# Performance work log

Measured on AMD Instinct MI355X. Metric: run time of the kernel, lower is better.

## Reference

```python
import jax, jax.numpy as jnp
import numpy as np

B, C, H, W = 8, 256, 64, 64
CK = 64  # C // k with k=4


def setup_inputs() -> dict:
    key = jax.random.key(0)
    ks = jax.random.split(key, 5)
    s = 1.0 / np.sqrt(C)
    return {
        "x": jax.random.normal(ks[0], (B, C, H, W), dtype=jnp.float32),
        "wq": jax.random.normal(ks[1], (CK, C), dtype=jnp.float32) * s,
        "bq": jnp.zeros((CK,), dtype=jnp.float32),
        "wk": jax.random.normal(ks[2], (CK, C), dtype=jnp.float32) * s,
        "bk": jnp.zeros((CK,), dtype=jnp.float32),
        "wv": jax.random.normal(ks[3], (C, C), dtype=jnp.float32) * s,
        "bv": jnp.zeros((C,), dtype=jnp.float32),
        "wg": jax.random.normal(ks[4], (C, C), dtype=jnp.float32) * s,
        "bg": jnp.zeros((C,), dtype=jnp.float32),
    }


def reference(x, wq, bq, wk, bk, wv, bv, wg, bg):
    b, c, h, w = x.shape
    n = h * w
    xf = x.reshape(b, c, n)  # [B, C, N]
    # 1x1 convs are channel-wise matmuls
    q = jnp.einsum('oc,bcn->bon', wq, xf) + bq[None, :, None]  # [B, Ck, N]
    k = jnp.einsum('oc,bcn->bon', wk, xf) + bk[None, :, None]  # [B, Ck, N]
    v = jnp.einsum('oc,bcn->bon', wv, xf) + bv[None, :, None]  # [B, C, N]
    # energy[b,i,j] = q[b,:,i] . k[b,:,j]
    energy = jnp.einsum('bci,bcj->bij', q, k)  # [B, N, N]
    energy = jax.nn.elu(energy) / n
    out = jnp.einsum('bcn,bnj->bcj', v, energy).reshape(b, c, h, w)
    out = jnp.einsum('oc,bchw->bohw', wg, out) + bg[None, :, None, None]
    return out
```

## Files before the change

kernel.cpp:

```cpp
#include <hip/hip_runtime.h>
#include <math.h>

#define BATCH 8
#define CH    256
#define NPIX  4096
#define CKDIM 64

typedef __attribute__((ext_vector_type(8))) short short8;
typedef __attribute__((ext_vector_type(4))) float f32x4;

#define MFMA16x16(a, b, c) __builtin_amdgcn_mfma_f32_16x16x32_bf16((a), (b), (c), 0, 0, 0)

__device__ __forceinline__ unsigned short f2bf(float f) {
    union { float f; unsigned int u; } v; v.f = f;
    unsigned int u = v.u;
    u += 0x7fffu + ((u >> 16) & 1u);
    return (unsigned short)(u >> 16);
}

__global__ void prep_kernel(const float* __restrict__ wq, const float* __restrict__ bq,
                            const float* __restrict__ wk, const float* __restrict__ bk,
                            const float* __restrict__ wv, const float* __restrict__ bv,
                            const float* __restrict__ wg,
                            unsigned short* __restrict__ W_all, float* __restrict__ bias_all) {
    int o = blockIdx.x;
    int c = threadIdx.x;
    if (o < 64) {
        W_all[o * CH + c] = f2bf(wq[o * CH + c]);
        if (c == 0) bias_all[o] = bq[o];
    } else if (o < 128) {
        int oo = o - 64;
        W_all[o * CH + c] = f2bf(wk[oo * CH + c]);
        if (c == 0) bias_all[o] = bk[oo];
    } else {
        int oo = o - 128;
        float acc = 0.f;
        for (int m = 0; m < CH; ++m)
            acc += wg[oo * CH + m] * wv[m * CH + c];
        W_all[o * CH + c] = f2bf(acc);
        if (c == 0) {
            float b = 0.f;
            for (int m = 0; m < CH; ++m) b += wg[oo * CH + m] * bv[m];
            bias_all[o] = b;
        }
    }
}

__global__ void xpose_kernel(const float* __restrict__ x, unsigned short* __restrict__ xt) {
    __shared__ float Tl[64][65];
    int n0 = blockIdx.x * 64;
    int c0 = blockIdx.y * 64;
    int b  = blockIdx.z;
    int tid = threadIdx.x;

#pragma unroll
    for (int r = 0; r < 4; ++r) {
        int f  = r * 256 + tid;
        int c  = f >> 4;
        int n4 = f & 15;
        float4 v = *(const float4*)(x + ((size_t)b * CH + c0 + c) * NPIX + n0 + n4 * 4);
        Tl[n4 * 4 + 0][c] = v.x;
        Tl[n4 * 4 + 1][c] = v.y;
        Tl[n4 * 4 + 2][c] = v.z;
        Tl[n4 * 4 + 3][c] = v.w;
    }
    __syncthreads();
#pragma unroll
    for (int r = 0; r < 2; ++r) {
        int f    = r * 256 + tid;
        int nrow = f >> 3;
        int c8   = f & 7;
        unsigned int pk[4];
#pragma unroll
        for (int p = 0; p < 4; ++p) {
            unsigned int lo = f2bf(Tl[nrow][c8 * 8 + p * 2 + 0]);
            unsigned int hi = f2bf(Tl[nrow][c8 * 8 + p * 2 + 1]);
            pk[p] = lo | (hi << 16);
        }
        *(uint4*)(xt + ((size_t)b * NPIX + n0 + nrow) * CH + c0 + c8 * 8) = *(uint4*)pk;
    }
}

__global__ void qkv_mfma(const unsigned short* __restrict__ xt,
                         const unsigned short* __restrict__ W_all,
                         const float* __restrict__ bias_all,
                         unsigned short* __restrict__ qk, unsigned short* __restrict__ vp) {
    __shared__ __align__(16) unsigned short Xl[64][264];

    int n0   = blockIdx.x * 64;
    int b    = blockIdx.y;
    int tid  = threadIdx.x;
    int lane = tid & 63;
    int w    = tid >> 6;
    int col  = lane & 15;
    int quad = lane >> 4;

#pragma unroll
    for (int r = 0; r < 8; ++r) {
        int f   = r * 256 + tid;
        int row = f >> 5;
        int c8  = f & 31;
        *(uint4*)&Xl[row][c8 * 8] = *(const uint4*)(xt + ((size_t)b * NPIX + n0 + row) * CH + c8 * 8);
    }
    __syncthreads();

#pragma unroll
    for (int og = 0; og < 6; ++og) {
        int o0 = og * 64;
        const unsigned short* Arow = W_all + (size_t)(o0 + w * 16 + col) * CH + quad * 8;

        f32x4 acc[4];
#pragma unroll
        for (int t = 0; t < 4; ++t) acc[t] = (f32x4){0.f, 0.f, 0.f, 0.f};

#pragma unroll
        for (int kc = 0; kc < 8; ++kc) {
            short8 a = *(const short8*)(Arow + kc * 32);
#pragma unroll
            for (int nt = 0; nt < 4; ++nt) {
                short8 bb = *(const short8*)&Xl[nt * 16 + col][kc * 32 + quad * 8];
                acc[nt] = MFMA16x16(a, bb, acc[nt]);
            }
        }

        float4 bias = *(const float4*)(bias_all + o0 + w * 16 + quad * 4);
        float bs[4] = {bias.x, bias.y, bias.z, bias.w};

        if (og < 2) {
#pragma unroll
            for (int nt = 0; nt < 4; ++nt) {
                int n = n0 + nt * 16 + col;
                unsigned int pk[2];
#pragma unroll
                for (int p = 0; p < 2; ++p) {
                    unsigned int lo = f2bf(acc[nt][p * 2 + 0] + bs[p * 2 + 0]);
                    unsigned int hi = f2bf(acc[nt][p * 2 + 1] + bs[p * 2 + 1]);
                    pk[p] = lo | (hi << 16);
                }
                *(uint2*)(qk + ((size_t)b * NPIX + n) * 128 + o0 + w * 16 + quad * 4) = *(uint2*)pk;
            }
        } else {
#pragma unroll
            for (int nt = 0; nt < 4; ++nt) {
                int n = n0 + nt * 16 + col;
#pragma unroll
                for (int r = 0; r < 4; ++r) {
                    int oo = o0 - 128 + w * 16 + quad * 4 + r;
                    vp[((size_t)b * CH + oo) * NPIX + n] = f2bf(acc[nt][r] + bs[r]);
                }
            }
        }
    }
}

#define LPK 72
__global__ __launch_bounds__(512, 4)
void attn_v4(const unsigned short* __restrict__ qk,
             const unsigned short* __restrict__ vp,
             const float* __restrict__ bg, float* __restrict__ out) {
    __shared__ __align__(16) unsigned short Qt[64][LPK];
    __shared__ __align__(16) unsigned short Vl[256][LPK];
    __shared__ __align__(16) unsigned short St[64][LPK];

    int j0   = blockIdx.x * 64;
    int b    = blockIdx.y;
    int tid  = threadIdx.x;
    int lane = tid & 63;
    int w    = tid >> 6;
    int col  = lane & 15;
    int quad = lane >> 4;

    int tjA = w & 3;
    int tiP = (w >> 2) * 2;

    short8 bK[2];
#pragma unroll
    for (int ks = 0; ks < 2; ++ks)
        bK[ks] = *(const short8*)(qk + ((size_t)b * NPIX + j0 + tjA * 16 + col) * 128 + 64 + ks * 32 + quad * 8);

    f32x4 acc[2][4];
#pragma unroll
    for (int ot = 0; ot < 2; ++ot)
#pragma unroll
        for (int tj = 0; tj < 4; ++tj) acc[ot][tj] = (f32x4){0.f, 0.f, 0.f, 0.f};

    for (int i0 = 0; i0 < NPIX; i0 += 64) {
        __syncthreads();

        {
            int row = tid >> 3, q8 = tid & 7;
            *(uint4*)&Qt[row][q8 * 8] =
                *(const uint4*)(qk + ((size_t)b * NPIX + i0 + row) * 128 + q8 * 8);
        }
#pragma unroll
        for (int r = 0; r < 4; ++r) {
            int f = r * 512 + tid;
            int row = f >> 3, q8 = f & 7;
            *(uint4*)&Vl[row][q8 * 8] =
                *(const uint4*)(vp + ((size_t)b * CH + row) * NPIX + i0 + q8 * 8);
        }
        __syncthreads();

#pragma unroll
        for (int t = 0; t < 2; ++t) {
            int ti = tiP + t;
            short8 a0 = *(const short8*)&Qt[ti * 16 + col][quad * 8];
            short8 a1 = *(const short8*)&Qt[ti * 16 + col][32 + quad * 8];
            f32x4 s = (f32x4){0.f, 0.f, 0.f, 0.f};
            s = MFMA16x16(a0, bK[0], s);
            s = MFMA16x16(a1, bK[1], s);
            unsigned int pk[2];
#pragma unroll
            for (int p = 0; p < 2; ++p) {
                float e0 = s[p * 2 + 0];
                float e1 = s[p * 2 + 1];
                e0 = (e0 > 0.f) ? e0 : (__expf(e0) - 1.f);
                e1 = (e1 > 0.f) ? e1 : (__expf(e1) - 1.f);
                e0 *= (1.f / (float)NPIX);
                e1 *= (1.f / (float)NPIX);
                pk[p] = (unsigned int)f2bf(e0) | ((unsigned int)f2bf(e1) << 16);
            }
            *(uint2*)&St[tjA * 16 + col][ti * 16 + quad * 4] = *(uint2*)pk;
        }
        __syncthreads();

#pragma unroll
        for (int ks = 0; ks < 2; ++ks) {
            short8 sb[4];
#pragma unroll
            for (int tj = 0; tj < 4; ++tj)
                sb[tj] = *(const short8*)&St[tj * 16 + col][ks * 32 + quad * 8];
#pragma unroll
            for (int ot = 0; ot < 2; ++ot) {
                short8 bv = *(const short8*)&Vl[(w * 2 + ot) * 16 + col][ks * 32 + quad * 8];
#pragma unroll
                for (int tj = 0; tj < 4; ++tj)
                    acc[ot][tj] = MFMA16x16(sb[tj], bv, acc[ot][tj]);
            }
        }
    }

#pragma unroll
    for (int ot = 0; ot < 2; ++ot) {
        int o = (w * 2 + ot) * 16 + col;
        float bgv = bg[o];
#pragma unroll
        for (int tj = 0; tj < 4; ++tj) {
            int j = j0 + tj * 16 + quad * 4;
            float4 st;
            st.x = acc[ot][tj][0] + bgv;
            st.y = acc[ot][tj][1] + bgv;
            st.z = acc[ot][tj][2] + bgv;
            st.w = acc[ot][tj][3] + bgv;
            *(float4*)&out[((size_t)b * CH + o) * NPIX + j] = st;
        }
    }
}

extern "C" void kernel_launch(void* const* d_in, const int* in_sizes, int n_in,
                              void* d_out, int out_size, void* d_ws, size_t ws_size,
                              hipStream_t stream) {
    const float* x  = (const float*)d_in[0];
    const float* wq = (const float*)d_in[1];
    const float* bq = (const float*)d_in[2];
    const float* wk = (const float*)d_in[3];
    const float* bk = (const float*)d_in[4];
    const float* wv = (const float*)d_in[5];
    const float* bv = (const float*)d_in[6];
    const float* wg = (const float*)d_in[7];
    const float* bg = (const float*)d_in[8];
    float* out = (float*)d_out;

    unsigned short* W_all = (unsigned short*)d_ws;
    float* bias_all = (float*)(W_all + 384 * 256);
    unsigned short* xt = (unsigned short*)(bias_all + 384);
    unsigned short* qk = xt + (size_t)BATCH * NPIX * CH;
    unsigned short* vp = qk + (size_t)BATCH * NPIX * 128;

    prep_kernel<<<dim3(384), dim3(256), 0, stream>>>(wq, bq, wk, bk, wv, bv, wg, W_all, bias_all);
    xpose_kernel<<<dim3(NPIX / 64, CH / 64, BATCH), dim3(256), 0, stream>>>(x, xt);
    qkv_mfma<<<dim3(NPIX / 64, BATCH), dim3(256), 0, stream>>>(xt, W_all, bias_all, qk, vp);
    attn_v4<<<dim3(NPIX / 64, BATCH), dim3(512), 0, stream>>>(qk, vp, bg, out);
}
```

Measured before the change: 265.9 us.

## Widen attention tile to 128 columns with double-buffered register-staged prefetch

The attention kernel now covers 128 output columns per block instead of 64. Each wave accumulates a 64x64 output tile, which halves how often the V and Q tiles are reloaded per output. The next Q/V tile is prefetched into registers during compute and written to a second LDS buffer, hiding global load latency. It also uses a hardware packed bf16 convert, a branch-free ELU, and raised wave priority around the MFMA loop. The cost is higher register and LDS use, with occupancy lowered to 2 blocks per CU, and only 256 blocks in the grid.

```diff
diff --git a/kernel.cpp b/kernel.cpp
--- a/kernel.cpp
+++ b/kernel.cpp
@@ -154,15 +154,15 @@
 }
 
 #define LPK 72
-__global__ __launch_bounds__(512, 4)
-void attn_v4(const unsigned short* __restrict__ qk,
+__global__ __launch_bounds__(512, 2)
+void attn_v5(const unsigned short* __restrict__ qk,
              const unsigned short* __restrict__ vp,
              const float* __restrict__ bg, float* __restrict__ out) {
-    __shared__ __align__(16) unsigned short Qt[64][LPK];
-    __shared__ __align__(16) unsigned short Vl[256][LPK];
-    __shared__ __align__(16) unsigned short St[64][LPK];
-
-    int j0   = blockIdx.x * 64;
+    __shared__ __align__(16) unsigned short Qt[2][64][LPK];
+    __shared__ __align__(16) unsigned short Vl[2][256][LPK];
+    __shared__ __align__(16) unsigned short St[128][LPK];
+
+    int j0   = blockIdx.x * 128;
     int b    = blockIdx.y;
     int tid  = threadIdx.x;
     int lane = tid & 63;
@@ -170,57 +170,85 @@
     int col  = lane & 15;
     int quad = lane >> 4;
 
-    int tjA = w & 3;
-    int tiP = (w >> 2) * 2;
-
-    short8 bK[2];
-#pragma unroll
-    for (int ks = 0; ks < 2; ++ks)
-        bK[ks] = *(const short8*)(qk + ((size_t)b * NPIX + j0 + tjA * 16 + col) * 128 + 64 + ks * 32 + quad * 8);
-
-    f32x4 acc[2][4];
-#pragma unroll
-    for (int ot = 0; ot < 2; ++ot)
-#pragma unroll
-        for (int tj = 0; tj < 4; ++tj) acc[ot][tj] = (f32x4){0.f, 0.f, 0.f, 0.f};
-
-    for (int i0 = 0; i0 < NPIX; i0 += 64) {
-        __syncthreads();
-
-        {
-            int row = tid >> 3, q8 = tid & 7;
-            *(uint4*)&Qt[row][q8 * 8] =
-                *(const uint4*)(qk + ((size_t)b * NPIX + i0 + row) * 128 + q8 * 8);
-        }
+    int wo  = w >> 1;
+    int wj  = w & 1;
+    int paj = w >> 1;
+    int pai = w & 1;
+
+    short8 bK[2][2];
+#pragma unroll
+    for (int jj = 0; jj < 2; ++jj) {
+        int jrow = j0 + (paj * 2 + jj) * 16 + col;
+#pragma unroll
+        for (int ks = 0; ks < 2; ++ks)
+            bK[jj][ks] = *(const short8*)(qk + ((size_t)b * NPIX + jrow) * 128 + 64 + ks * 32 + quad * 8);
+    }
+
+    f32x4 acc[4][4];
+#pragma unroll
+    for (int ot = 0; ot < 4; ++ot)
+#pragma unroll
+        for (int jt = 0; jt < 4; ++jt) acc[ot][jt] = (f32x4){0.f, 0.f, 0.f, 0.f};
+
+    {
+        int row = tid >> 3, q8 = tid & 7;
+        uint4 q0 = *(const uint4*)(qk + ((size_t)b * NPIX + row) * 128 + q8 * 8);
+        *(uint4*)&Qt[0][row][q8 * 8] = q0;
 #pragma unroll
         for (int r = 0; r < 4; ++r) {
             int f = r * 512 + tid;
-            int row = f >> 3, q8 = f & 7;
-            *(uint4*)&Vl[row][q8 * 8] =
-                *(const uint4*)(vp + ((size_t)b * CH + row) * NPIX + i0 + q8 * 8);
-        }
+            uint4 v0 = *(const uint4*)(vp + ((size_t)b * CH + (f >> 3)) * NPIX + (f & 7) * 8);
+            *(uint4*)&Vl[0][f >> 3][(f & 7) * 8] = v0;
+        }
+    }
+
+    const float invN = 1.f / (float)NPIX;
+    uint4 vr[4]; uint4 qr;
+
+    for (int it = 0; it < NPIX / 64; ++it) {
+        int p = it & 1;
+        int more = (it + 1) < (NPIX / 64);
+        int inext = (it + 1) * 64;
+
+        if (more) {
+            int row = tid >> 3, q8 = tid & 7;
+            qr = *(const uint4*)(qk + ((size_t)b * NPIX + inext + row) * 128 + q8 * 8);
+#pragma unroll
+            for (int r = 0; r < 4; ++r) {
+                int f = r * 512 + tid;
+                vr[r] = *(const uint4*)(vp + ((size_t)b * CH + (f >> 3)) * NPIX + inext + (f & 7) * 8);
+            }
+        }
+
         __syncthreads();
 
 #pragma unroll
-        for (int t = 0; t < 2; ++t) {
-            int ti = tiP + t;
-            short8 a0 = *(const short8*)&Qt[ti * 16 + col][quad * 8];
-            short8 a1 = *(const short8*)&Qt[ti * 16 + col][32 + quad * 8];
-            f32x4 s = (f32x4){0.f, 0.f, 0.f, 0.f};
-            s = MFMA16x16(a0, bK[0], s);
-            s = MFMA16x16(a1, bK[1], s);
-            unsigned int pk[2];
-#pragma unroll
-            for (int p = 0; p < 2; ++p) {
-                float e0 = s[p * 2 + 0];
-                float e1 = s[p * 2 + 1];
-                e0 = (e0 > 0.f) ? e0 : (__expf(e0) - 1.f);
-                e1 = (e1 > 0.f) ? e1 : (__expf(e1) - 1.f);
-                e0 *= (1.f / (float)NPIX);
-                e1 *= (1.f / (float)NPIX);
-                pk[p] = (unsigned int)f2bf(e0) | ((unsigned int)f2bf(e1) << 16);
-            }
-            *(uint2*)&St[tjA * 16 + col][ti * 16 + quad * 4] = *(uint2*)pk;
+        for (int ii = 0; ii < 2; ++ii) {
+            int isub = pai * 2 + ii;
+            short8 a0 = *(const short8*)&Qt[p][isub * 16 + col][quad * 8];
+            short8 a1 = *(const short8*)&Qt[p][isub * 16 + col][32 + quad * 8];
+#pragma unroll
+            for (int jj = 0; jj < 2; ++jj) {
+                f32x4 s = (f32x4){0.f, 0.f, 0.f, 0.f};
+                s = MFMA16x16(a0, bK[jj][0], s);
+                s = MFMA16x16(a1, bK[jj][1], s);
+                unsigned int pk2[2];
+#pragma unroll
+                for (int pp = 0; pp < 2; ++pp) {
+                    float e0 = s[pp * 2 + 0];
+                    float e1 = s[pp * 2 + 1];
+                    float g0 = __expf(e0) - 1.f;
+                    float g1 = __expf(e1) - 1.f;
+                    e0 = (e0 > 0.f) ? e0 : g0;
+                    e1 = (e1 > 0.f) ? e1 : g1;
+                    e0 *= invN;
+                    e1 *= invN;
+                    unsigned int rpk;
+                    asm("v_cvt_pk_bf16_f32 %0, %1, %2" : "=v"(rpk) : "v"(e0), "v"(e1));
+                    pk2[pp] = rpk;
+                }
+                *(uint2*)&St[(paj * 2 + jj) * 16 + col][isub * 16 + quad * 4] = *(uint2*)pk2;
+            }
         }
         __syncthreads();
 
@@ -228,30 +256,43 @@
         for (int ks = 0; ks < 2; ++ks) {
             short8 sb[4];
 #pragma unroll
-            for (int tj = 0; tj < 4; ++tj)
-                sb[tj] = *(const short8*)&St[tj * 16 + col][ks * 32 + quad * 8];
-#pragma unroll
-            for (int ot = 0; ot < 2; ++ot) {
-                short8 bv = *(const short8*)&Vl[(w * 2 + ot) * 16 + col][ks * 32 + quad * 8];
-#pragma unroll
-                for (int tj = 0; tj < 4; ++tj)
-                    acc[ot][tj] = MFMA16x16(sb[tj], bv, acc[ot][tj]);
-            }
-        }
-    }
-
-#pragma unroll
-    for (int ot = 0; ot < 2; ++ot) {
-        int o = (w * 2 + ot) * 16 + col;
+            for (int jt = 0; jt < 4; ++jt)
+                sb[jt] = *(const short8*)&St[wj * 64 + jt * 16 + col][ks * 32 + quad * 8];
+#pragma unroll
+            for (int ot = 0; ot < 4; ++ot) {
+                short8 vb = *(const short8*)&Vl[p][wo * 64 + ot * 16 + col][ks * 32 + quad * 8];
+                __builtin_amdgcn_s_setprio(1);
+#pragma unroll
+                for (int jt = 0; jt < 4; ++jt)
+                    acc[ot][jt] = MFMA16x16(sb[jt], vb, acc[ot][jt]);
+                __builtin_amdgcn_s_setprio(0);
+            }
+        }
+
+        if (more) {
+            int pn = p ^ 1;
+            int row = tid >> 3, q8 = tid & 7;
+            *(uint4*)&Qt[pn][row][q8 * 8] = qr;
+#pragma unroll
+            for (int r = 0; r < 4; ++r) {
+                int f = r * 512 + tid;
+                *(uint4*)&Vl[pn][f >> 3][(f & 7) * 8] = vr[r];
+            }
+        }
+    }
+
+#pragma unroll
+    for (int ot = 0; ot < 4; ++ot) {
+        int o = wo * 64 + ot * 16 + col;
         float bgv = bg[o];
 #pragma unroll
-        for (int tj = 0; tj < 4; ++tj) {
-            int j = j0 + tj * 16 + quad * 4;
+        for (int jt = 0; jt < 4; ++jt) {
+            int j = j0 + wj * 64 + jt * 16 + quad * 4;
             float4 st;
-            st.x = acc[ot][tj][0] + bgv;
-            st.y = acc[ot][tj][1] + bgv;
-            st.z = acc[ot][tj][2] + bgv;
-            st.w = acc[ot][tj][3] + bgv;
+            st.x = acc[ot][jt][0] + bgv;
+            st.y = acc[ot][jt][1] + bgv;
+            st.z = acc[ot][jt][2] + bgv;
+            st.w = acc[ot][jt][3] + bgv;
             *(float4*)&out[((size_t)b * CH + o) * NPIX + j] = st;
         }
     }
@@ -280,5 +321,5 @@
     prep_kernel<<<dim3(384), dim3(256), 0, stream>>>(wq, bq, wk, bk, wv, bv, wg, W_all, bias_all);
     xpose_kernel<<<dim3(NPIX / 64, CH / 64, BATCH), dim3(256), 0, stream>>>(x, xt);
     qkv_mfma<<<dim3(NPIX / 64, BATCH), dim3(256), 0, stream>>>(xt, W_all, bias_all, qk, vp);
-    attn_v4<<<dim3(NPIX / 64, BATCH), dim3(512), 0, stream>>>(qk, vp, bg, out);
-}
+    attn_v5<<<dim3(NPIX / 128, BATCH), dim3(512), 0, stream>>>(qk, vp, bg, out);
+}
```

Measured after the change: 305.5 us. 14.9% more time.

## Prefetch Q and V into registers, drop V LDS staging, interleave batch blocks

Applied to the files above, without the earlier changes.

The attention kernel no longer stages V through shared memory. Each lane loads its own V MFMA operand fragments straight from global memory into registers, and the next tile's Q and V are prefetched into registers while the current tile is computed, which removes one barrier per iteration. Block indices are remapped so consecutive blocks cover different batches, the ELU conversion uses the hardware packed bf16 convert with branchless exp, and s_setprio is raised around the MFMA burst. These changes cut LDS traffic and expose load latency overlap, at the cost of higher register pressure and uncoalesced per-lane global V loads.

```diff
diff --git a/kernel.cpp b/kernel.cpp
--- a/kernel.cpp
+++ b/kernel.cpp
@@ -155,15 +155,15 @@
 
 #define LPK 72
 __global__ __launch_bounds__(512, 4)
-void attn_v4(const unsigned short* __restrict__ qk,
+void attn_v6(const unsigned short* __restrict__ qk,
              const unsigned short* __restrict__ vp,
              const float* __restrict__ bg, float* __restrict__ out) {
     __shared__ __align__(16) unsigned short Qt[64][LPK];
-    __shared__ __align__(16) unsigned short Vl[256][LPK];
     __shared__ __align__(16) unsigned short St[64][LPK];
 
-    int j0   = blockIdx.x * 64;
-    int b    = blockIdx.y;
+    int lin  = blockIdx.y * gridDim.x + blockIdx.x;
+    int b    = lin & 7;
+    int j0   = (lin >> 3) * 64;
     int tid  = threadIdx.x;
     int lane = tid & 63;
     int w    = tid >> 6;
@@ -184,21 +184,35 @@
 #pragma unroll
         for (int tj = 0; tj < 4; ++tj) acc[ot][tj] = (f32x4){0.f, 0.f, 0.f, 0.f};
 
+    int qrow = tid >> 3, q8 = tid & 7;
+    const unsigned short* Qsrc = qk + ((size_t)b * NPIX + qrow) * 128 + q8 * 8;
+    const unsigned short* Vsrc[2];
+#pragma unroll
+    for (int ot = 0; ot < 2; ++ot)
+        Vsrc[ot] = vp + ((size_t)b * CH + (w * 2 + ot) * 16 + col) * NPIX + quad * 8;
+
+    uint4 qr = *(const uint4*)Qsrc;
+    short8 vb[2][2];
+#pragma unroll
+    for (int ot = 0; ot < 2; ++ot)
+#pragma unroll
+        for (int ks = 0; ks < 2; ++ks)
+            vb[ot][ks] = *(const short8*)(Vsrc[ot] + ks * 32);
+
+    const float invN = 1.f / (float)NPIX;
+
     for (int i0 = 0; i0 < NPIX; i0 += 64) {
-        __syncthreads();
-
-        {
-            int row = tid >> 3, q8 = tid & 7;
-            *(uint4*)&Qt[row][q8 * 8] =
-                *(const uint4*)(qk + ((size_t)b * NPIX + i0 + row) * 128 + q8 * 8);
-        }
-#pragma unroll
-        for (int r = 0; r < 4; ++r) {
-            int f = r * 512 + tid;
-            int row = f >> 3, q8 = f & 7;
-            *(uint4*)&Vl[row][q8 * 8] =
-                *(const uint4*)(vp + ((size_t)b * CH + row) * NPIX + i0 + q8 * 8);
-        }
+        *(uint4*)&Qt[qrow][q8 * 8] = qr;
+
+        int inext = (i0 + 64) & (NPIX - 1);
+        uint4 qr_n = *(const uint4*)(Qsrc + (size_t)inext * 128);
+        short8 vb_n[2][2];
+#pragma unroll
+        for (int ot = 0; ot < 2; ++ot)
+#pragma unroll
+            for (int ks = 0; ks < 2; ++ks)
+                vb_n[ot][ks] = *(const short8*)(Vsrc[ot] + inext + ks * 32);
+
         __syncthreads();
 
 #pragma unroll
@@ -209,18 +223,22 @@
             f32x4 s = (f32x4){0.f, 0.f, 0.f, 0.f};
             s = MFMA16x16(a0, bK[0], s);
             s = MFMA16x16(a1, bK[1], s);
-            unsigned int pk[2];
-#pragma unroll
-            for (int p = 0; p < 2; ++p) {
-                float e0 = s[p * 2 + 0];
-                float e1 = s[p * 2 + 1];
-                e0 = (e0 > 0.f) ? e0 : (__expf(e0) - 1.f);
-                e1 = (e1 > 0.f) ? e1 : (__expf(e1) - 1.f);
-                e0 *= (1.f / (float)NPIX);
-                e1 *= (1.f / (float)NPIX);
-                pk[p] = (unsigned int)f2bf(e0) | ((unsigned int)f2bf(e1) << 16);
+            unsigned int pk2[2];
+#pragma unroll
+            for (int pp = 0; pp < 2; ++pp) {
+                float e0 = s[pp * 2 + 0];
+                float e1 = s[pp * 2 + 1];
+                float g0 = __expf(e0) - 1.f;
+                float g1 = __expf(e1) - 1.f;
+                e0 = (e0 > 0.f) ? e0 : g0;
+                e1 = (e1 > 0.f) ? e1 : g1;
+                e0 *= invN;
+                e1 *= invN;
+                unsigned int rpk;
+                asm("v_cvt_pk_bf16_f32 %0, %1, %2" : "=v"(rpk) : "v"(e0), "v"(e1));
+                pk2[pp] = rpk;
             }
-            *(uint2*)&St[tjA * 16 + col][ti * 16 + quad * 4] = *(uint2*)pk;
+            *(uint2*)&St[tjA * 16 + col][ti * 16 + quad * 4] = *(uint2*)pk2;
         }
         __syncthreads();
 
@@ -230,14 +248,21 @@
 #pragma unroll
             for (int tj = 0; tj < 4; ++tj)
                 sb[tj] = *(const short8*)&St[tj * 16 + col][ks * 32 + quad * 8];
-#pragma unroll
-            for (int ot = 0; ot < 2; ++ot) {
-                short8 bv = *(const short8*)&Vl[(w * 2 + ot) * 16 + col][ks * 32 + quad * 8];
+            __builtin_amdgcn_s_setprio(1);
+#pragma unroll
+            for (int ot = 0; ot < 2; ++ot)
 #pragma unroll
                 for (int tj = 0; tj < 4; ++tj)
-                    acc[ot][tj] = MFMA16x16(sb[tj], bv, acc[ot][tj]);
-            }
-        }
+                    acc[ot][tj] = MFMA16x16(sb[tj], vb[ot][ks], acc[ot][tj]);
+            __builtin_amdgcn_s_setprio(0);
+        }
+
+        qr = qr_n;
+#pragma unroll
+        for (int ot = 0; ot < 2; ++ot)
+#pragma unroll
+            for (int ks = 0; ks < 2; ++ks)
+                vb[ot][ks] = vb_n[ot][ks];
     }
 
 #pragma unroll
@@ -280,5 +305,5 @@
     prep_kernel<<<dim3(384), dim3(256), 0, stream>>>(wq, bq, wk, bk, wv, bv, wg, W_all, bias_all);
     xpose_kernel<<<dim3(NPIX / 64, CH / 64, BATCH), dim3(256), 0, stream>>>(x, xt);
     qkv_mfma<<<dim3(NPIX / 64, BATCH), dim3(256), 0, stream>>>(xt, W_all, bias_all, qk, vp);
-    attn_v4<<<dim3(NPIX / 64, BATCH), dim3(512), 0, stream>>>(qk, vp, bg, out);
-}
+    attn_v6<<<dim3(NPIX / 64, BATCH), dim3(512), 0, stream>>>(qk, vp, bg, out);
+}
```

After: 266.0 us. About the same (+0.0%).
